# Optimization experiments

Hardware: AMD Instinct MI355X
Metric: run time of the kernel (lower is better)

## Reference

```python
import jax, jax.numpy as jnp
import numpy as np

BETA = 0.25      # commitment loss weight
DECAY = 0.99     # EMA decay
EPS = 1e-5       # Laplace smoothing for counts


def setup_inputs() -> dict:
    key = jax.random.key(0)
    k1, k2, k3 = jax.random.split(key, 3)
    B, d, h, w, K = 16, 64, 64, 64, 1024
    z_e = jax.random.normal(k1, (B, d, h, w), dtype=jnp.float32)
    codebook = jax.random.normal(k2, (K, d), dtype=jnp.float32)
    ema_count = jnp.ones((K,), dtype=jnp.float32)
    ema_sum = jax.random.normal(k3, (K, d), dtype=jnp.float32)
    return {"z_e": z_e, "codebook": codebook, "ema_count": ema_count, "ema_sum": ema_sum}


def reference(z_e, codebook, ema_count, ema_sum):
    B, d, h, w = z_e.shape
    K = codebook.shape[0]
    # [B,d,h,w] -> [N,d], N = B*h*w
    z_flat = jnp.transpose(z_e, (0, 2, 3, 1)).reshape(-1, d)
    # squared euclidean distances [N,K]
    dist = (jnp.sum(z_flat * z_flat, axis=1, keepdims=True)
            - 2.0 * (z_flat @ codebook.T)
            + jnp.sum(codebook * codebook, axis=1)[None, :])
    indices = jnp.argmin(dist, axis=1)                      # [N] int
    e_k = codebook[indices].reshape(B, h, w, d).transpose(0, 3, 1, 2)  # [B,d,h,w]

    # --- EMA codebook update (training mode, no grad) ---
    zf = jax.lax.stop_gradient(z_flat)
    counts = jax.ops.segment_sum(jnp.ones((zf.shape[0],), dtype=zf.dtype), indices, num_segments=K)
    sums = jax.ops.segment_sum(zf, indices, num_segments=K)
    new_count = ema_count * DECAY + (1.0 - DECAY) * counts
    new_sum = ema_sum * DECAY + (1.0 - DECAY) * sums
    n = jnp.sum(new_count)
    count_s = (new_count + EPS) / (n + K * EPS) * n
    new_codebook = new_sum / count_s[:, None]

    # straight-through estimator
    e_k_ste = z_e + jax.lax.stop_gradient(e_k - z_e)
    L_commit = (jnp.mean((z_e - jax.lax.stop_gradient(e_k)) ** 2)
                + BETA * jnp.mean((jax.lax.stop_gradient(z_e) - e_k) ** 2))
    return (e_k_ste, indices.reshape(B, h, w), L_commit, new_codebook, new_count, new_sum)
```

## Files before the change

kernel.cpp:

```cpp
#include <hip/hip_runtime.h>
#include <hip/hip_bf16.h>
#include <hip/hip_fp16.h>

#define NB 16
#define DD 64
#define HW 4096
#define NTOT 65536
#define KC 1024

#define O_EK   0
#define O_IDX  4194304
#define O_L    4259840
#define O_CB   4259841
#define O_CNT  4325377
#define O_SUM  4326401

#define WS_IDX    0
#define WS_LCPART 65536
#define WS_N      66048
#define WS_CNORM  66560
#define WS_PSUM   67584
#define WS_PCNT   329728
#define WS_ZN     333824
#define WS_CBH    399360
#define WS_CBL    432128

#define MARGIN 0.002f
#define FLAGBIT 0x40000000

typedef _Float16 v8h __attribute__((ext_vector_type(8)));
typedef float    v4f __attribute__((ext_vector_type(4)));

__global__ __launch_bounds__(256) void k_pre(const float* __restrict__ cb,
                                             const float* __restrict__ ema_count,
                                             float* __restrict__ cnorm,
                                             float* __restrict__ n_ws,
                                             unsigned short* __restrict__ cbh,
                                             unsigned short* __restrict__ cbl) {
    const int t = threadIdx.x;
    const int w = (blockIdx.x * 256 + t) >> 6;
    const int l = t & 63;
    float s = 0.f;
    if (l < 16) {
        float4 v = *(const float4*)(cb + (size_t)w * DD + l * 4);
        s = v.x * v.x + v.y * v.y + v.z * v.z + v.w * v.w;
    }
#pragma unroll
    for (int m = 1; m <= 8; m <<= 1) s += __shfl_xor(s, m, 64);
    if (l == 0) cnorm[w] = s;

    const int e4 = blockIdx.x * 256 + t;
    if (e4 < 16384) {
        float4 v4 = ((const float4*)cb)[e4];
        __half hx = __float2half(v4.x), hy = __float2half(v4.y),
               hz = __float2half(v4.z), hw2 = __float2half(v4.w);
        ushort4 h4 = { __half_as_ushort(hx), __half_as_ushort(hy),
                       __half_as_ushort(hz), __half_as_ushort(hw2) };
        ((ushort4*)cbh)[e4] = h4;
        ushort4 l4 = { __half_as_ushort(__float2half(v4.x - __half2float(hx))),
                       __half_as_ushort(__float2half(v4.y - __half2float(hy))),
                       __half_as_ushort(__float2half(v4.z - __half2float(hz))),
                       __half_as_ushort(__float2half(v4.w - __half2float(hw2))) };
        ((ushort4*)cbl)[e4] = l4;
    }

    if (blockIdx.x == 0) {
        __shared__ float red[256];
        red[t] = ema_count[t] + ema_count[t + 256] + ema_count[t + 512] + ema_count[t + 768];
        __syncthreads();
        for (int s2 = 128; s2 >= 1; s2 >>= 1) {
            if (t < s2) red[t] += red[t + s2];
            __syncthreads();
        }
        if (t == 0) n_ws[0] = 0.99f * red[0] + 0.01f * 65536.0f;
    }
}

__global__ __launch_bounds__(256) void k_argmin(const float* __restrict__ z_e,
                                                const unsigned short* __restrict__ cbh,
                                                const unsigned short* __restrict__ cbl,
                                                const float* __restrict__ cnorm,
                                                int* __restrict__ idx_ws,
                                                float* __restrict__ zn_ws) {
    __shared__ __align__(16) unsigned short Ah[128 * 72];
    __shared__ __align__(16) unsigned short Al[128 * 72];
    __shared__ __align__(16) unsigned short Bh[128 * 72];
    __shared__ __align__(16) unsigned short Bl[128 * 72];
    __shared__ __align__(16) float cn_lds[KC];

    const int t  = threadIdx.x;
    const int n0 = blockIdx.x * 128;
    const int b   = n0 >> 12;
    const int hw0 = n0 & 4095;

    *(float4*)&cn_lds[t * 4] = *(const float4*)(cnorm + t * 4);

    if (t < 128) {
        const float* zp = z_e + (size_t)b * (DD * HW) + hw0 + t;
        float s = 0.f;
        unsigned ph = 0, pl = 0;
        for (int j = 0; j < 64; ++j) {
            float v = zp[(size_t)j * HW];
            s = fmaf(v, v, s);
            __half h = __float2half(v);
            float hf = __half2float(h);
            __half lo = __float2half(v - hf);
            unsigned uh = __half_as_ushort(h), ul = __half_as_ushort(lo);
            if ((j & 1) == 0) { ph = uh; pl = ul; }
            else {
                *(unsigned*)&Ah[t * 72 + j - 1] = ph | (uh << 16);
                *(unsigned*)&Al[t * 72 + j - 1] = pl | (ul << 16);
            }
        }
        zn_ws[n0 + t] = s;
    }
    __syncthreads();

    const int w    = t >> 6;
    const int lane = t & 63;
    const int c    = lane & 15;
    const int q    = lane >> 4;

    v8h Afh[2][2], Afl[2][2];
#pragma unroll
    for (int g = 0; g < 2; ++g) {
        int m = 32 * w + 16 * g + c;
#pragma unroll
        for (int s = 0; s < 2; ++s) {
            Afh[g][s] = *(const v8h*)&Ah[m * 72 + s * 32 + q * 8];
            Afl[g][s] = *(const v8h*)&Al[m * 72 + s * 32 + q * 8];
        }
    }

    float m1v[2][4], m2v[2][4]; int m1i[2][4];
#pragma unroll
    for (int g = 0; g < 2; ++g)
#pragma unroll
        for (int r = 0; r < 4; ++r) { m1v[g][r] = 3.4e38f; m2v[g][r] = 3.4e38f; m1i[g][r] = 0; }

    for (int kt = 0; kt < 8; ++kt) {
        __syncthreads();
#pragma unroll
        for (int s2 = 0; s2 < 4; ++s2) {
            int idx = t + s2 * 256;
            int code = idx >> 3;
            int off  = (idx & 7) * 8;
            size_t gsrc = ((size_t)(kt * 128 + code)) * 64 + off;
            *(uint4*)&Bh[code * 72 + off] = *(const uint4*)(cbh + gsrc);
            *(uint4*)&Bl[code * 72 + off] = *(const uint4*)(cbl + gsrc);
        }
        __syncthreads();

#pragma unroll
        for (int sub = 0; sub < 8; ++sub) {
            const int cl = sub * 16 + c;
            v8h Bfh0 = *(const v8h*)&Bh[cl * 72 + q * 8];
            v8h Bfh1 = *(const v8h*)&Bh[cl * 72 + 32 + q * 8];
            v8h Bfl0 = *(const v8h*)&Bl[cl * 72 + q * 8];
            v8h Bfl1 = *(const v8h*)&Bl[cl * 72 + 32 + q * 8];
            float cnc = cn_lds[kt * 128 + cl];
            const int kg = kt * 128 + cl;
#pragma unroll
            for (int g = 0; g < 2; ++g) {
                v4f acc = {0.f, 0.f, 0.f, 0.f};
                acc = __builtin_amdgcn_mfma_f32_16x16x32_f16(Afh[g][0], Bfh0, acc, 0, 0, 0);
                acc = __builtin_amdgcn_mfma_f32_16x16x32_f16(Afh[g][1], Bfh1, acc, 0, 0, 0);
                acc = __builtin_amdgcn_mfma_f32_16x16x32_f16(Afh[g][0], Bfl0, acc, 0, 0, 0);
                acc = __builtin_amdgcn_mfma_f32_16x16x32_f16(Afh[g][1], Bfl1, acc, 0, 0, 0);
                acc = __builtin_amdgcn_mfma_f32_16x16x32_f16(Afl[g][0], Bfh0, acc, 0, 0, 0);
                acc = __builtin_amdgcn_mfma_f32_16x16x32_f16(Afl[g][1], Bfh1, acc, 0, 0, 0);
#pragma unroll
                for (int r = 0; r < 4; ++r) {
                    float v = fmaf(-2.0f, acc[r], cnc);
                    bool better = v < m1v[g][r];
                    m2v[g][r] = better ? m1v[g][r] : fminf(m2v[g][r], v);
                    m1i[g][r] = better ? kg : m1i[g][r];
                    m1v[g][r] = better ? v : m1v[g][r];
                }
            }
        }
    }

#pragma unroll
    for (int g = 0; g < 2; ++g)
#pragma unroll
        for (int r = 0; r < 4; ++r) {
            float a = m1v[g][r], b2 = m2v[g][r]; int ii = m1i[g][r];
#pragma unroll
            for (int mask = 1; mask <= 8; mask <<= 1) {
                float ov = __shfl_xor(a, mask, 64);
                int   oi = __shfl_xor(ii, mask, 64);
                float o2 = __shfl_xor(b2, mask, 64);
                bool take = (ov < a) || (ov == a && oi < ii);
                float loser = take ? a : ov;
                b2 = fminf(fminf(b2, o2), loser);
                a  = take ? ov : a;
                ii = take ? oi : ii;
            }
            if (c == 0) {
                int row = 32 * w + 16 * g + q * 4 + r;
                int enc = ((b2 - a) < MARGIN) ? (ii | FLAGBIT) : ii;
                idx_ws[n0 + row] = enc;
            }
        }
}

__global__ __launch_bounds__(256) void k_scatter(const float* __restrict__ z_e,
                                                 const float* __restrict__ cb,
                                                 const float* __restrict__ cnorm,
                                                 const float* __restrict__ zn_ws,
                                                 int* __restrict__ idx_ws,
                                                 float* __restrict__ out,
                                                 float* __restrict__ lc_part) {
    __shared__ int idx_lds[128];
    __shared__ int flagrows[128];
    __shared__ int nflag;
    __shared__ float redv[256];
    __shared__ int   redi[256];
    __shared__ float lcred[4];

    const int t  = threadIdx.x;
    const int n0 = blockIdx.x * 128;
    const int b   = n0 >> 12;
    const int hw0 = n0 & 4095;

    if (t == 0) nflag = 0;
    __syncthreads();
    if (t < 128) {
        int raw = idx_ws[n0 + t];
        idx_lds[t] = raw & 1023;
        if (raw & FLAGBIT) { int p = atomicAdd(&nflag, 1); flagrows[p] = t; }
    }
    __syncthreads();
    const int nf = nflag;
    for (int f = 0; f < nf; ++f) {
        int row = flagrows[f];
        int n = n0 + row;
        const float* zp = z_e + (size_t)b * (DD * HW) + (hw0 + row);
        float znr = zn_ws[n];
        float best = 3.4e38f; int bi = 0;
#pragma unroll
        for (int c2 = 0; c2 < 4; ++c2) {
            int k = t * 4 + c2;
            const float* ck = cb + (size_t)k * DD;
            float acc = 0.f;
            for (int j = 0; j < 64; ++j) acc = fmaf(zp[(size_t)j * HW], ck[j], acc);
            float v = (znr - 2.0f * acc) + cnorm[k];
            if (v < best) { best = v; bi = k; }
        }
        redv[t] = best; redi[t] = bi;
        __syncthreads();
        for (int s = 128; s >= 1; s >>= 1) {
            if (t < s) {
                float v = redv[t + s]; int i = redi[t + s];
                if (v < redv[t] || (v == redv[t] && i < redi[t])) { redv[t] = v; redi[t] = i; }
            }
            __syncthreads();
        }
        if (t == 0) { idx_lds[row] = redi[0]; idx_ws[n] = redi[0]; }
        __syncthreads();
    }

    if (t < 128) out[O_IDX + n0 + t] = (float)idx_lds[t];

    const int r  = t >> 1;
    const int j0 = (t & 1) * 32;
    int k = idx_lds[r];
    const float* ck = cb + (size_t)k * DD;
    const float* zb = z_e + (size_t)b * (DD * HW) + (hw0 + r);
    const size_t obase = (size_t)b * (DD * HW) + (size_t)(hw0 + r);

    float lc = 0.f;
#pragma unroll 8
    for (int j = j0; j < j0 + 32; ++j) {
        float z = zb[(size_t)j * HW];
        float e = ck[j];
        out[O_EK + obase + (size_t)j * HW] = z + (e - z);
        float d = z - e;
        lc = fmaf(d, d, lc);
    }
#pragma unroll
    for (int m = 32; m >= 1; m >>= 1) lc += __shfl_xor(lc, m, 64);
    if ((t & 63) == 0) lcred[t >> 6] = lc;
    __syncthreads();
    if (t == 0) lc_part[blockIdx.x] = lcred[0] + lcred[1] + lcred[2] + lcred[3];
}

__global__ __launch_bounds__(1024) void k_sums(const int* __restrict__ idx_ws,
                                               const float* __restrict__ z_e,
                                               float* __restrict__ psum,
                                               int* __restrict__ pcnt) {
    __shared__ float acc[KC];
    __shared__ int bins[KC];
    const int j = blockIdx.x & 63;
    const int c = blockIdx.x >> 6;
    const int t = threadIdx.x;
    acc[t] = 0.f;
    bins[t] = 0;
    __syncthreads();
    const float* zj = z_e + (size_t)j * HW;
    const int base = c * 16384;
    if (j == 0) {
#pragma unroll
        for (int i = 0; i < 4; ++i) {
            int n4 = base + i * 4096 + t * 4;
            int b = n4 >> 12, hw = n4 & 4095;
            float4 z4 = *(const float4*)(zj + (size_t)b * (DD * HW) + hw);
            int4   k4 = *(const int4*)(idx_ws + n4);
            atomicAdd(&acc[k4.x], z4.x); atomicAdd(&bins[k4.x], 1);
            atomicAdd(&acc[k4.y], z4.y); atomicAdd(&bins[k4.y], 1);
            atomicAdd(&acc[k4.z], z4.z); atomicAdd(&bins[k4.z], 1);
            atomicAdd(&acc[k4.w], z4.w); atomicAdd(&bins[k4.w], 1);
        }
    } else {
#pragma unroll
        for (int i = 0; i < 4; ++i) {
            int n4 = base + i * 4096 + t * 4;
            int b = n4 >> 12, hw = n4 & 4095;
            float4 z4 = *(const float4*)(zj + (size_t)b * (DD * HW) + hw);
            int4   k4 = *(const int4*)(idx_ws + n4);
            atomicAdd(&acc[k4.x], z4.x);
            atomicAdd(&acc[k4.y], z4.y);
            atomicAdd(&acc[k4.z], z4.z);
            atomicAdd(&acc[k4.w], z4.w);
        }
    }
    __syncthreads();
    psum[(size_t)c * 65536 + j * 1024 + t] = acc[t];
    if (j == 0) pcnt[c * 1024 + t] = bins[t];
}

__global__ __launch_bounds__(1024) void k_epi(const float* __restrict__ psum,
                                              const int* __restrict__ pcnt,
                                              const float* __restrict__ ema_sum,
                                              const float* __restrict__ ema_count,
                                              const float* __restrict__ n_ws,
                                              const float* __restrict__ lc_part,
                                              float* __restrict__ out) {
    const int t = threadIdx.x;
    const int e = blockIdx.x * 1024 + t;
    const int k = e >> 6, j = e & 63;
    float s4 = psum[j * 1024 + k] + psum[65536 + j * 1024 + k]
             + psum[131072 + j * 1024 + k] + psum[196608 + j * 1024 + k];
    float ns = ema_sum[e] * 0.99f + 0.01f * s4;
    out[O_SUM + e] = ns;
    int cnt = pcnt[k] + pcnt[1024 + k] + pcnt[2048 + k] + pcnt[3072 + k];
    float nc = ema_count[k] * 0.99f + 0.01f * (float)cnt;
    float n  = n_ws[0];
    float cs = (nc + 1e-5f) / (n + 1024.0f * 1e-5f) * n;
    out[O_CB + e] = ns / cs;
    if (blockIdx.x == 0) {
        int c2 = pcnt[t] + pcnt[1024 + t] + pcnt[2048 + t] + pcnt[3072 + t];
        out[O_CNT + t] = ema_count[t] * 0.99f + 0.01f * (float)c2;
    }
    if (blockIdx.x == 1) {
        __shared__ float red[512];
        if (t < 512) red[t] = lc_part[t];
        __syncthreads();
        for (int s = 256; s >= 1; s >>= 1) {
            if (t < s) red[t] += red[t + s];
            __syncthreads();
        }
        if (t == 0) out[O_L] = 1.25f * red[0] * (1.0f / 4194304.0f);
    }
}

extern "C" void kernel_launch(void* const* d_in, const int* in_sizes, int n_in,
                              void* d_out, int out_size, void* d_ws, size_t ws_size,
                              hipStream_t stream) {
    const float* z_e       = (const float*)d_in[0];
    const float* cb        = (const float*)d_in[1];
    const float* ema_count = (const float*)d_in[2];
    const float* ema_sum   = (const float*)d_in[3];
    float* out             = (float*)d_out;

    float* ws_f      = (float*)d_ws;
    int*   idx_ws    = (int*)d_ws;
    float* lc_part   = ws_f + WS_LCPART;
    float* n_ws      = ws_f + WS_N;
    float* cnorm_ws  = ws_f + WS_CNORM;
    float* psum      = ws_f + WS_PSUM;
    int*   pcnt      = (int*)(ws_f + WS_PCNT);
    float* zn_ws     = ws_f + WS_ZN;
    unsigned short* cbh = (unsigned short*)(ws_f + WS_CBH);
    unsigned short* cbl = (unsigned short*)(ws_f + WS_CBL);

    k_pre<<<256, 256, 0, stream>>>(cb, ema_count, cnorm_ws, n_ws, cbh, cbl);
    k_argmin<<<NTOT / 128, 256, 0, stream>>>(z_e, cbh, cbl, cnorm_ws, idx_ws, zn_ws);
    k_scatter<<<NTOT / 128, 256, 0, stream>>>(z_e, cb, cnorm_ws, zn_ws, idx_ws, out, lc_part);
    k_sums<<<256, 1024, 0, stream>>>(idx_ws, z_e, psum, pcnt);
    k_epi<<<64, 1024, 0, stream>>>(psum, pcnt, ema_sum, ema_count, n_ws, lc_part, out);
}
```

Measured before the change: 170.4 us.

## Fuse argmin and scatter kernels, stage z tile in LDS as fp32

Merges the scatter/refinement/commit-loss kernel into the argmin kernel so each block keeps its 128-row z tile in shared memory as fp32. The tile is loaded once with coalesced float4 loads and reused for the norm, the split-fp16 MMA fragments, the exact recheck of ambiguous rows and the e_k output. This removes a second full read of z_e, the zn and flag round trips through global memory, and one launch. The cost is more LDS per block (a 32KB fp32 tile), which may lower occupancy, plus strided LDS reads when building the fragments.

```diff
diff --git a/kernel.cpp b/kernel.cpp
--- a/kernel.cpp
+++ b/kernel.cpp
@@ -21,12 +21,10 @@
 #define WS_CNORM  66560
 #define WS_PSUM   67584
 #define WS_PCNT   329728
-#define WS_ZN     333824
 #define WS_CBH    399360
 #define WS_CBL    432128
 
 #define MARGIN 0.002f
-#define FLAGBIT 0x40000000
 
 typedef _Float16 v8h __attribute__((ext_vector_type(8)));
 typedef float    v4f __attribute__((ext_vector_type(4)));
@@ -77,42 +75,48 @@
 }
 
 __global__ __launch_bounds__(256) void k_argmin(const float* __restrict__ z_e,
+                                                const float* __restrict__ cb,
                                                 const unsigned short* __restrict__ cbh,
                                                 const unsigned short* __restrict__ cbl,
                                                 const float* __restrict__ cnorm,
                                                 int* __restrict__ idx_ws,
-                                                float* __restrict__ zn_ws) {
-    __shared__ __align__(16) unsigned short Ah[128 * 72];
-    __shared__ __align__(16) unsigned short Al[128 * 72];
+                                                float* __restrict__ out,
+                                                float* __restrict__ lc_part) {
+    __shared__ __align__(16) float At[64 * 128];
     __shared__ __align__(16) unsigned short Bh[128 * 72];
     __shared__ __align__(16) unsigned short Bl[128 * 72];
     __shared__ __align__(16) float cn_lds[KC];
+    __shared__ float znl[128];
+    __shared__ int   idx_lds[128];
+    __shared__ int   flagrows[128];
+    __shared__ int   nflag;
+    __shared__ float redv[256];
+    __shared__ int   redi[256];
+    __shared__ float lcred[4];
 
     const int t  = threadIdx.x;
     const int n0 = blockIdx.x * 128;
     const int b   = n0 >> 12;
     const int hw0 = n0 & 4095;
-
+    const float* zbase = z_e + (size_t)b * (DD * HW) + hw0;
+
+    if (t == 0) nflag = 0;
     *(float4*)&cn_lds[t * 4] = *(const float4*)(cnorm + t * 4);
 
+#pragma unroll
+    for (int s = 0; s < 8; ++s) {
+        int idx = t + s * 256;
+        int j   = idx >> 5;
+        int i4  = (idx & 31) << 2;
+        float4 v = *(const float4*)(zbase + (size_t)j * HW + i4);
+        *(float4*)(&At[j * 128 + i4]) = v;
+    }
+    __syncthreads();
+
     if (t < 128) {
-        const float* zp = z_e + (size_t)b * (DD * HW) + hw0 + t;
         float s = 0.f;
-        unsigned ph = 0, pl = 0;
-        for (int j = 0; j < 64; ++j) {
-            float v = zp[(size_t)j * HW];
-            s = fmaf(v, v, s);
-            __half h = __float2half(v);
-            float hf = __half2float(h);
-            __half lo = __float2half(v - hf);
-            unsigned uh = __half_as_ushort(h), ul = __half_as_ushort(lo);
-            if ((j & 1) == 0) { ph = uh; pl = ul; }
-            else {
-                *(unsigned*)&Ah[t * 72 + j - 1] = ph | (uh << 16);
-                *(unsigned*)&Al[t * 72 + j - 1] = pl | (ul << 16);
-            }
-        }
-        zn_ws[n0 + t] = s;
+        for (int j = 0; j < 64; ++j) { float a = At[j * 128 + t]; s = fmaf(a, a, s); }
+        znl[t] = s;
     }
     __syncthreads();
 
@@ -127,8 +131,15 @@
         int m = 32 * w + 16 * g + c;
 #pragma unroll
         for (int s = 0; s < 2; ++s) {
-            Afh[g][s] = *(const v8h*)&Ah[m * 72 + s * 32 + q * 8];
-            Afl[g][s] = *(const v8h*)&Al[m * 72 + s * 32 + q * 8];
+            v8h hi, lo;
+#pragma unroll
+            for (int jj = 0; jj < 8; ++jj) {
+                float v = At[(s * 32 + q * 8 + jj) * 128 + m];
+                _Float16 h = (_Float16)v;
+                hi[jj] = h;
+                lo[jj] = (_Float16)(v - (float)h);
+            }
+            Afh[g][s] = hi; Afl[g][s] = lo;
         }
     }
 
@@ -199,53 +210,24 @@
             }
             if (c == 0) {
                 int row = 32 * w + 16 * g + q * 4 + r;
-                int enc = ((b2 - a) < MARGIN) ? (ii | FLAGBIT) : ii;
-                idx_ws[n0 + row] = enc;
-            }
-        }
-}
-
-__global__ __launch_bounds__(256) void k_scatter(const float* __restrict__ z_e,
-                                                 const float* __restrict__ cb,
-                                                 const float* __restrict__ cnorm,
-                                                 const float* __restrict__ zn_ws,
-                                                 int* __restrict__ idx_ws,
-                                                 float* __restrict__ out,
-                                                 float* __restrict__ lc_part) {
-    __shared__ int idx_lds[128];
-    __shared__ int flagrows[128];
-    __shared__ int nflag;
-    __shared__ float redv[256];
-    __shared__ int   redi[256];
-    __shared__ float lcred[4];
-
-    const int t  = threadIdx.x;
-    const int n0 = blockIdx.x * 128;
-    const int b   = n0 >> 12;
-    const int hw0 = n0 & 4095;
-
-    if (t == 0) nflag = 0;
-    __syncthreads();
-    if (t < 128) {
-        int raw = idx_ws[n0 + t];
-        idx_lds[t] = raw & 1023;
-        if (raw & FLAGBIT) { int p = atomicAdd(&nflag, 1); flagrows[p] = t; }
-    }
-    __syncthreads();
+                idx_lds[row] = ii;
+                if ((b2 - a) < MARGIN) { int p = atomicAdd(&nflag, 1); flagrows[p] = row; }
+            }
+        }
+    __syncthreads();
+
     const int nf = nflag;
     for (int f = 0; f < nf; ++f) {
         int row = flagrows[f];
-        int n = n0 + row;
-        const float* zp = z_e + (size_t)b * (DD * HW) + (hw0 + row);
-        float znr = zn_ws[n];
+        float znr = znl[row];
         float best = 3.4e38f; int bi = 0;
 #pragma unroll
         for (int c2 = 0; c2 < 4; ++c2) {
             int k = t * 4 + c2;
             const float* ck = cb + (size_t)k * DD;
             float acc = 0.f;
-            for (int j = 0; j < 64; ++j) acc = fmaf(zp[(size_t)j * HW], ck[j], acc);
-            float v = (znr - 2.0f * acc) + cnorm[k];
+            for (int j = 0; j < 64; ++j) acc = fmaf(At[j * 128 + row], ck[j], acc);
+            float v = (znr - 2.0f * acc) + cn_lds[k];
             if (v < best) { best = v; bi = k; }
         }
         redv[t] = best; redi[t] = bi;
@@ -257,23 +239,27 @@
             }
             __syncthreads();
         }
-        if (t == 0) { idx_lds[row] = redi[0]; idx_ws[n] = redi[0]; }
-        __syncthreads();
-    }
-
-    if (t < 128) out[O_IDX + n0 + t] = (float)idx_lds[t];
+        if (t == 0) idx_lds[row] = redi[0];
+        __syncthreads();
+    }
+
+    if (t < 128) {
+        int bi = idx_lds[t];
+        out[O_IDX + n0 + t] = (float)bi;
+        idx_ws[n0 + t] = bi;
+    }
+    __syncthreads();
 
     const int r  = t >> 1;
     const int j0 = (t & 1) * 32;
     int k = idx_lds[r];
     const float* ck = cb + (size_t)k * DD;
-    const float* zb = z_e + (size_t)b * (DD * HW) + (hw0 + r);
     const size_t obase = (size_t)b * (DD * HW) + (size_t)(hw0 + r);
 
     float lc = 0.f;
 #pragma unroll 8
     for (int j = j0; j < j0 + 32; ++j) {
-        float z = zb[(size_t)j * HW];
+        float z = At[j * 128 + r];
         float e = ck[j];
         out[O_EK + obase + (size_t)j * HW] = z + (e - z);
         float d = z - e;
@@ -381,13 +367,11 @@
     float* cnorm_ws  = ws_f + WS_CNORM;
     float* psum      = ws_f + WS_PSUM;
     int*   pcnt      = (int*)(ws_f + WS_PCNT);
-    float* zn_ws     = ws_f + WS_ZN;
     unsigned short* cbh = (unsigned short*)(ws_f + WS_CBH);
     unsigned short* cbl = (unsigned short*)(ws_f + WS_CBL);
 
     k_pre<<<256, 256, 0, stream>>>(cb, ema_count, cnorm_ws, n_ws, cbh, cbl);
-    k_argmin<<<NTOT / 128, 256, 0, stream>>>(z_e, cbh, cbl, cnorm_ws, idx_ws, zn_ws);
-    k_scatter<<<NTOT / 128, 256, 0, stream>>>(z_e, cb, cnorm_ws, zn_ws, idx_ws, out, lc_part);
+    k_argmin<<<NTOT / 128, 256, 0, stream>>>(z_e, cb, cbh, cbl, cnorm_ws, idx_ws, out, lc_part);
     k_sums<<<256, 1024, 0, stream>>>(idx_ws, z_e, psum, pcnt);
     k_epi<<<64, 1024, 0, stream>>>(psum, pcnt, ema_sum, ema_count, n_ws, lc_part, out);
 }
```

New measurement: 188.0 us. 1.1x slower.
